# Kernel tuning notes

Measured on AMD Instinct MI355X. Metric: run time of the kernel, lower is better.

## Reference

```python
import jax, jax.numpy as jnp
import numpy as np

B, BARS, BEATS, FRAC = 64, 16, 4, 8
IN_F = 10 * 47 * 2  # 940
LIN_OUT = 100
BEAT_H = 16
BAR_H = 32


def _p(key, shape, scale=0.05):
    return jax.random.normal(key, shape, dtype=jnp.float32) * scale


def setup_inputs() -> dict:
    key = jax.random.key(0)
    ks = jax.random.split(key, 16)
    return {
        "channels": jax.random.normal(ks[0], (B, BARS, BEATS, FRAC, 10, 2, 47), dtype=jnp.float32),
        "lin_w": _p(ks[1], (LIN_OUT, IN_F)),
        "lin_b": _p(ks[2], (LIN_OUT,)),
        # beats LSTM (unidirectional), PyTorch gate order i,f,g,o
        "b_wih": _p(ks[3], (4 * BEAT_H, LIN_OUT)),
        "b_whh": _p(ks[4], (4 * BEAT_H, BEAT_H)),
        "b_bih": _p(ks[5], (4 * BEAT_H,)),
        "b_bhh": _p(ks[6], (4 * BEAT_H,)),
        # bars LSTM, bidirectional: forward (f_) and reverse (r_) directions
        "f_wih": _p(ks[7], (4 * BAR_H, BEAT_H)),
        "f_whh": _p(ks[8], (4 * BAR_H, BAR_H)),
        "f_bih": _p(ks[9], (4 * BAR_H,)),
        "f_bhh": _p(ks[10], (4 * BAR_H,)),
        "r_wih": _p(ks[11], (4 * BAR_H, BEAT_H)),
        "r_whh": _p(ks[12], (4 * BAR_H, BAR_H)),
        "r_bih": _p(ks[13], (4 * BAR_H,)),
        "r_bhh": _p(ks[14], (4 * BAR_H,)),
    }


def lstm(x, wih, whh, bih, bhh):
    """PyTorch-semantics LSTM, batch_first. x: [N, T, F] -> h_seq [N, T, H]."""
    N = x.shape[0]
    H = whh.shape[1]
    # precompute input contribution for all timesteps
    xg = jnp.einsum('ntf,gf->ntg', x, wih) + (bih + bhh)  # [N, T, 4H]

    def step(carry, xt):
        h, c = carry
        gates = xt + h @ whh.T  # [N, 4H]
        i, f, g, o = jnp.split(gates, 4, axis=-1)
        c = jax.nn.sigmoid(f) * c + jax.nn.sigmoid(i) * jnp.tanh(g)
        h = jax.nn.sigmoid(o) * jnp.tanh(c)
        return (h, c), h

    h0 = jnp.zeros((N, H), x.dtype)
    _, hs = jax.lax.scan(step, (h0, h0), jnp.swapaxes(xg, 0, 1))  # [T, N, H]
    return jnp.swapaxes(hs, 0, 1)


def bilstm(x, f_wih, f_whh, f_bih, f_bhh, r_wih, r_whh, r_bih, r_bhh):
    fwd = lstm(x, f_wih, f_whh, f_bih, f_bhh)
    bwd = jnp.flip(lstm(jnp.flip(x, axis=1), r_wih, r_whh, r_bih, r_bhh), axis=1)
    return jnp.concatenate([fwd, bwd], axis=-1)


def reference(channels, lin_w, lin_b,
              b_wih, b_whh, b_bih, b_bhh,
              f_wih, f_whh, f_bih, f_bhh,
              r_wih, r_whh, r_bih, r_bhh):
    # channels: [B, bars, beats, frac, 10, 2, 47]
    x = jnp.swapaxes(channels, -1, -2)  # [..., 10, 47, 2]
    x = x.reshape(*x.shape[:4], IN_F)   # squash dims 4..6 -> 940
    x = jax.nn.relu(x @ lin_w.T + lin_b)  # [B, bars, beats, frac, 100]

    # Distributed depth=2: fold (B, bars, beats) into batch, seq over frac
    xb = x.reshape(B * BARS * BEATS, FRAC, LIN_OUT)
    beats = lstm(xb, b_wih, b_whh, b_bih, b_bhh)
    beats = beats.reshape(B, BARS, BEATS, FRAC, BEAT_H)

    # last fraction hidden state, then Distributed depth=1 over beats axis
    xl = beats[:, :, :, -1].reshape(B * BARS, BEATS, BEAT_H)
    bars = bilstm(xl, f_wih, f_whh, f_bih, f_bhh, r_wih, r_whh, r_bih, r_bhh)
    bars = bars.reshape(B, BARS, BEATS, 2 * BAR_H)
    return beats, bars
```

## Files before the change

### kernel.cpp

```cpp
#include <hip/hip_runtime.h>
#include <hip/hip_bf16.h>

typedef float f32x4 __attribute__((ext_vector_type(4)));
typedef short bf16x8 __attribute__((ext_vector_type(8)));

#define MFMA16(a, b, c) __builtin_amdgcn_mfma_f32_16x16x32_bf16(a, b, c, 0, 0, 0)

constexpr int K1  = 940;
constexpr int KP2 = 1024;
constexpr int NP  = 112;
constexpr int OSL = 136;
constexpr int BSR = 136;
constexpr int BUFE = NP * BSR;

__device__ __forceinline__ float sigf(float x) { return 1.f / (1.f + __expf(-x)); }
__device__ __forceinline__ float tanhfast(float x) { return 2.f / (1.f + __expf(-2.f * x)) - 1.f; }

__device__ __forceinline__ short f2b(float x) {
  __hip_bfloat16 b = __float2bfloat16(x);
  return *reinterpret_cast<short*>(&b);
}

__global__ void prep_kernel(const float* __restrict__ lin_w,
                            const float* __restrict__ b_wih,
                            __hip_bfloat16* __restrict__ w2,
                            __hip_bfloat16* __restrict__ bw2) {
  int idx = blockIdx.x * 256 + threadIdx.x;
  if (idx < NP * KP2) {
    int n = idx >> 10, k = idx & 1023;
    float v = 0.f;
    if (n < 100 && k < K1) {
      int c10 = k / 94, rem = k - c10 * 94;
      int c2 = rem / 47, c47 = rem - c2 * 47;
      int f = c10 * 94 + c47 * 2 + c2;
      v = lin_w[n * K1 + f];
    }
    w2[idx] = __float2bfloat16(v);
  } else {
    int i2 = idx - NP * KP2;
    if (i2 < 64 * 128) {
      int g = i2 >> 7, k = i2 & 127;
      bw2[i2] = __float2bfloat16((k < 100) ? b_wih[g * 100 + k] : 0.f);
    }
  }
}

__global__ __launch_bounds__(256, 2)
void fused_encoder(const float* __restrict__ ch,
                   const __hip_bfloat16* __restrict__ w2,
                   const float* __restrict__ lin_b,
                   const __hip_bfloat16* __restrict__ bw2,
                   const float* __restrict__ bih,
                   const float* __restrict__ bhh,
                   const float* __restrict__ whh,
                   const float* __restrict__ fwih, const float* __restrict__ fwhh,
                   const float* __restrict__ fbih, const float* __restrict__ fbhh,
                   const float* __restrict__ rwih, const float* __restrict__ rwhh,
                   const float* __restrict__ rbih, const float* __restrict__ rbhh,
                   float* __restrict__ beats,
                   float* __restrict__ bars) {
  __shared__ __align__(16) char smem[2 * BUFE * 2];
  __hip_bfloat16* Bs    = reinterpret_cast<__hip_bfloat16*>(smem);
  __hip_bfloat16* out_s = reinterpret_cast<__hip_bfloat16*>(smem);
  float*          xg_s  = reinterpret_cast<float*>(smem + 17408);
  float (*hlast)[16]    = reinterpret_cast<float(*)[16]>(smem + 34048);
  float (*hb)[32]       = reinterpret_cast<float(*)[32]>(smem + 34560);
  float (*gact)[128]    = reinterpret_cast<float(*)[128]>(smem + 34816);

  const int tid = threadIdx.x;
  const int w = tid >> 6, lane = tid & 63;
  const int l16 = lane & 15, bq = lane >> 4;

  const int mbase = blockIdx.x * 64 + w * 16;
  const float* ar = ch + (long)(mbase + l16) * K1 + bq * 8;

  float lb[7];
#pragma unroll
  for (int nt = 0; nt < 7; ++nt) {
    int col = nt * 16 + l16;
    lb[nt] = (col < 100) ? lin_b[col] : 0.f;
  }

  auto mk = [&](float4 lo, float4 hi) -> bf16x8 {
    return bf16x8{f2b(lo.x), f2b(lo.y), f2b(lo.z), f2b(lo.w),
                  f2b(hi.x), f2b(hi.y), f2b(hi.z), f2b(hi.w)};
  };

  f32x4 acc[7] = {};
  float4 Ab[2][8];
  bf16x8 bst[8];

  const float4 f40{0.f, 0.f, 0.f, 0.f};
  auto ldA = [&](int c, float4* d) {
    const float* p = ar + c * 128;
    if (c < 7) {
#pragma unroll
      for (int ks = 0; ks < 4; ++ks) {
        d[2 * ks]     = *reinterpret_cast<const float4*>(p + ks * 32);
        d[2 * ks + 1] = *reinterpret_cast<const float4*>(p + ks * 32 + 4);
      }
    } else {
      d[0] = *reinterpret_cast<const float4*>(p);
      d[1] = *reinterpret_cast<const float4*>(p + 4);
      d[2] = (bq <= 1) ? *reinterpret_cast<const float4*>(p + 32) : f40;
      d[3] = (bq == 0) ? *reinterpret_cast<const float4*>(p + 36) : f40;
      d[4] = d[5] = d[6] = d[7] = f40;
    }
  };

  const int sn = tid >> 1, kh = (tid & 1) * 64;
  auto stageB_ld = [&](int c) {
    if (sn < NP) {
      const __hip_bfloat16* src = w2 + sn * KP2 + c * 128 + kh;
#pragma unroll
      for (int j = 0; j < 8; ++j)
        bst[j] = *reinterpret_cast<const bf16x8*>(src + j * 8);
    }
  };
  auto stageB_st = [&](int buf) {
    if (sn < NP) {
      __hip_bfloat16* dst = Bs + buf * BUFE + sn * BSR + kh;
#pragma unroll
      for (int j = 0; j < 8; ++j)
        *reinterpret_cast<bf16x8*>(dst + j * 8) = bst[j];
    }
  };

  stageB_ld(0);
  stageB_st(0);
  ldA(0, Ab[0]);
  __syncthreads();

  for (int c = 0; c < 8; ++c) {
    if (c < 7) {
      stageB_ld(c + 1);
      ldA(c + 1, Ab[(c + 1) & 1]);
    }
    const __hip_bfloat16* Bc = Bs + (c & 1) * BUFE;
    float4* A = Ab[c & 1];
#pragma unroll
    for (int ks = 0; ks < 4; ++ks) {
      bf16x8 bf[7];
#pragma unroll
      for (int nt = 0; nt < 7; ++nt)
        bf[nt] = *reinterpret_cast<const bf16x8*>(
            &Bc[(nt * 16 + l16) * BSR + ks * 32 + bq * 8]);
      bf16x8 a = mk(A[2 * ks], A[2 * ks + 1]);
#pragma unroll
      for (int nt = 0; nt < 7; ++nt) acc[nt] = MFMA16(a, bf[nt], acc[nt]);
    }
    if (c < 7) stageB_st((c + 1) & 1);
    __syncthreads();
  }

#pragma unroll
  for (int nt = 0; nt < 7; ++nt) {
    const int col = nt * 16 + l16;
#pragma unroll
    for (int r = 0; r < 4; ++r) {
      float v = fmaxf(acc[nt][r] + lb[nt], 0.f);
      out_s[(w * 16 + bq * 4 + r) * OSL + col] = __float2bfloat16((col < 100) ? v : 0.f);
    }
  }
#pragma unroll
  for (int r = 0; r < 4; ++r)
    out_s[(w * 16 + bq * 4 + r) * OSL + 112 + l16] = __float2bfloat16(0.f);

  {
    bf16x8 av[4];
#pragma unroll
    for (int s = 0; s < 4; ++s)
      av[s] = *reinterpret_cast<const bf16x8*>(&out_s[(w * 16 + l16) * OSL + s * 32 + bq * 8]);
    f32x4 xacc[4] = {};
#pragma unroll
    for (int gt = 0; gt < 4; ++gt) {
#pragma unroll
      for (int s = 0; s < 4; ++s) {
        bf16x8 b = *reinterpret_cast<const bf16x8*>(&bw2[(gt * 16 + l16) * 128 + s * 32 + bq * 8]);
        xacc[gt] = MFMA16(av[s], b, xacc[gt]);
      }
    }
#pragma unroll
    for (int gt = 0; gt < 4; ++gt) {
      const int gate = gt * 16 + l16;
      const float bias = bih[gate] + bhh[gate];
#pragma unroll
      for (int r = 0; r < 4; ++r)
        xg_s[(w * 16 + bq * 4 + r) * 65 + gate] = xacc[gt][r] + bias;
    }
  }

  {
    const int cell = lane & 15;
    float wr[16];
#pragma unroll
    for (int u = 0; u < 16; ++u) wr[u] = whh[lane * 16 + u];
    float xv0[8], xv1[8];
#pragma unroll
    for (int t = 0; t < 8; ++t) {
      xv0[t] = xg_s[(w * 16 + t) * 65 + lane];
      xv1[t] = xg_s[(w * 16 + 8 + t) * 65 + lane];
    }
    float h0[16], h1[16];
#pragma unroll
    for (int u = 0; u < 16; ++u) { h0[u] = 0.f; h1[u] = 0.f; }
    float c0 = 0.f, c1 = 0.f;
    const long sg0 = (long)blockIdx.x * 8 + 2 * w;
    const long sg1 = sg0 + 1;
#pragma unroll
    for (int t = 0; t < 8; ++t) {
      float p0 = xv0[t], p1 = xv1[t];
#pragma unroll
      for (int u = 0; u < 16; ++u) { p0 += wr[u] * h0[u]; p1 += wr[u] * h1[u]; }
      const bool istanh = (lane >= 32 && lane < 48);
      float a0 = istanh ? tanhfast(p0) : sigf(p0);
      float a1 = istanh ? tanhfast(p1) : sigf(p1);
      float gi0 = __shfl(a0, cell),      gi1 = __shfl(a1, cell);
      float gf0 = __shfl(a0, cell + 16), gf1 = __shfl(a1, cell + 16);
      float gg0 = __shfl(a0, cell + 32), gg1 = __shfl(a1, cell + 32);
      float go0 = __shfl(a0, cell + 48), go1 = __shfl(a1, cell + 48);
      c0 = gf0 * c0 + gi0 * gg0;
      c1 = gf1 * c1 + gi1 * gg1;
      float hn0 = go0 * tanhfast(c0);
      float hn1 = go1 * tanhfast(c1);
#pragma unroll
      for (int u = 0; u < 16; ++u) { h0[u] = __shfl(hn0, u); h1[u] = __shfl(hn1, u); }
      if (lane < 16) {
        beats[sg0 * 128 + t * 16 + lane] = hn0;
        beats[sg1 * 128 + t * 16 + lane] = hn1;
        if (t == 7) {
          hlast[2 * w][lane]     = hn0;
          hlast[2 * w + 1][lane] = hn1;
        }
      }
    }
  }
  __syncthreads();

  {
    const int dir = tid >> 7, g = tid & 127;
    const float* wihp = dir ? rwih : fwih;
    const float* whhp = dir ? rwhh : fwhh;
    const float bias = dir ? (rbih[g] + rbhh[g]) : (fbih[g] + fbhh[g]);
    float wi[16], wh[32];
#pragma unroll
    for (int u = 0; u < 16; ++u) wi[u] = wihp[g * 16 + u];
#pragma unroll
    for (int u = 0; u < 32; ++u) wh[u] = whhp[g * 32 + u];
    for (int b2 = 0; b2 < 2; ++b2) {
      const int n = blockIdx.x * 2 + b2;
      float c = 0.f;
      if (g < 32) hb[dir][g] = 0.f;
      __syncthreads();
      for (int t = 0; t < 4; ++t) {
        const int tt = dir ? (3 - t) : t;
        float pre = bias;
#pragma unroll
        for (int u = 0; u < 16; ++u) pre += wi[u] * hlast[b2 * 4 + tt][u];
#pragma unroll
        for (int u = 0; u < 32; ++u) pre += wh[u] * hb[dir][u];
        gact[dir][g] = (g >= 64 && g < 96) ? tanhfast(pre) : sigf(pre);
        __syncthreads();
        if (g < 32) {
          c = gact[dir][32 + g] * c + gact[dir][g] * gact[dir][64 + g];
          float hn = gact[dir][96 + g] * tanhfast(c);
          hb[dir][g] = hn;
          bars[(n * 4 + tt) * 64 + dir * 32 + g] = hn;
        }
        __syncthreads();
      }
    }
  }
}

extern "C" void kernel_launch(void* const* d_in, const int* in_sizes, int n_in,
                              void* d_out, int out_size, void* d_ws, size_t ws_size,
                              hipStream_t stream) {
  const float* ch    = (const float*)d_in[0];
  const float* lin_w = (const float*)d_in[1];
  const float* lin_b = (const float*)d_in[2];
  const float* b_wih = (const float*)d_in[3];
  const float* b_whh = (const float*)d_in[4];
  const float* b_bih = (const float*)d_in[5];
  const float* b_bhh = (const float*)d_in[6];
  const float* f_wih = (const float*)d_in[7];
  const float* f_whh = (const float*)d_in[8];
  const float* f_bih = (const float*)d_in[9];
  const float* f_bhh = (const float*)d_in[10];
  const float* r_wih = (const float*)d_in[11];
  const float* r_whh = (const float*)d_in[12];
  const float* r_bih = (const float*)d_in[13];
  const float* r_bhh = (const float*)d_in[14];

  char* ws = (char*)d_ws;
  __hip_bfloat16* w2  = (__hip_bfloat16*)ws;
  __hip_bfloat16* bw2 = (__hip_bfloat16*)(ws + 229376);
  float*          out = (float*)d_out;

  prep_kernel<<<480, 256, 0, stream>>>(lin_w, b_wih, w2, bw2);
  fused_encoder<<<512, 256, 0, stream>>>(ch, w2, lin_b, bw2, b_bih, b_bhh,
                                         b_whh,
                                         f_wih, f_whh, f_bih, f_bhh,
                                         r_wih, r_whh, r_bih, r_bhh,
                                         out, out + 524288);
}
```

Measured before the change: 227.9 us.

## Split fused encoder into split-K linear GEMM and separate LSTM kernel

Splits the fused kernel into two kernels. The first is a linear GEMM over 2048 blocks of 16 rows, where each of the four waves handles a quarter of K, loads B fragments straight from global memory with no LDS staging, and reduces the partial sums through shared memory. The second is a separate LSTM kernel that reads the bf16 linear activations from a workspace buffer. The goal is more parallelism and occupancy for the memory-bound GEMM, which reads about 123MB of input. The cost is an extra kernel launch and a global round-trip for the intermediate activations.

```diff
diff --git a/kernel.cpp b/kernel.cpp
--- a/kernel.cpp
+++ b/kernel.cpp
@@ -10,8 +10,6 @@
 constexpr int KP2 = 1024;
 constexpr int NP  = 112;
 constexpr int OSL = 136;
-constexpr int BSR = 136;
-constexpr int BUFE = NP * BSR;
 
 __device__ __forceinline__ float sigf(float x) { return 1.f / (1.f + __expf(-x)); }
 __device__ __forceinline__ float tanhfast(float x) { return 2.f / (1.f + __expf(-2.f * x)) - 1.f; }
@@ -19,6 +17,11 @@
 __device__ __forceinline__ short f2b(float x) {
   __hip_bfloat16 b = __float2bfloat16(x);
   return *reinterpret_cast<short*>(&b);
+}
+
+__device__ __forceinline__ bf16x8 mk8(float4 lo, float4 hi) {
+  return bf16x8{f2b(lo.x), f2b(lo.y), f2b(lo.z), f2b(lo.w),
+                f2b(hi.x), f2b(hi.y), f2b(hi.z), f2b(hi.w)};
 }
 
 __global__ void prep_kernel(const float* __restrict__ lin_w,
@@ -45,126 +48,110 @@
   }
 }
 
-__global__ __launch_bounds__(256, 2)
-void fused_encoder(const float* __restrict__ ch,
-                   const __hip_bfloat16* __restrict__ w2,
-                   const float* __restrict__ lin_b,
-                   const __hip_bfloat16* __restrict__ bw2,
-                   const float* __restrict__ bih,
-                   const float* __restrict__ bhh,
-                   const float* __restrict__ whh,
-                   const float* __restrict__ fwih, const float* __restrict__ fwhh,
-                   const float* __restrict__ fbih, const float* __restrict__ fbhh,
-                   const float* __restrict__ rwih, const float* __restrict__ rwhh,
-                   const float* __restrict__ rbih, const float* __restrict__ rbhh,
-                   float* __restrict__ beats,
-                   float* __restrict__ bars) {
-  __shared__ __align__(16) char smem[2 * BUFE * 2];
-  __hip_bfloat16* Bs    = reinterpret_cast<__hip_bfloat16*>(smem);
-  __hip_bfloat16* out_s = reinterpret_cast<__hip_bfloat16*>(smem);
-  float*          xg_s  = reinterpret_cast<float*>(smem + 17408);
-  float (*hlast)[16]    = reinterpret_cast<float(*)[16]>(smem + 34048);
-  float (*hb)[32]       = reinterpret_cast<float(*)[32]>(smem + 34560);
-  float (*gact)[128]    = reinterpret_cast<float(*)[128]>(smem + 34816);
-
+__global__ __launch_bounds__(256)
+void linear_gemm(const float* __restrict__ ch,
+                 const __hip_bfloat16* __restrict__ w2,
+                 const float* __restrict__ lin_b,
+                 __hip_bfloat16* __restrict__ out1) {
+  __shared__ float red[4][16][116];
   const int tid = threadIdx.x;
   const int w = tid >> 6, lane = tid & 63;
   const int l16 = lane & 15, bq = lane >> 4;
-
-  const int mbase = blockIdx.x * 64 + w * 16;
-  const float* ar = ch + (long)(mbase + l16) * K1 + bq * 8;
-
-  float lb[7];
-#pragma unroll
-  for (int nt = 0; nt < 7; ++nt) {
-    int col = nt * 16 + l16;
-    lb[nt] = (col < 100) ? lin_b[col] : 0.f;
-  }
-
-  auto mk = [&](float4 lo, float4 hi) -> bf16x8 {
-    return bf16x8{f2b(lo.x), f2b(lo.y), f2b(lo.z), f2b(lo.w),
-                  f2b(hi.x), f2b(hi.y), f2b(hi.z), f2b(hi.w)};
-  };
+  const int mbase = blockIdx.x * 16;
+  const int wkb = w * 256;
+  const float* ar = ch + (long)(mbase + l16) * K1 + wkb + bq * 8;
 
   f32x4 acc[7] = {};
-  float4 Ab[2][8];
-  bf16x8 bst[8];
-
-  const float4 f40{0.f, 0.f, 0.f, 0.f};
-  auto ldA = [&](int c, float4* d) {
-    const float* p = ar + c * 128;
-    if (c < 7) {
-#pragma unroll
-      for (int ks = 0; ks < 4; ++ks) {
-        d[2 * ks]     = *reinterpret_cast<const float4*>(p + ks * 32);
-        d[2 * ks + 1] = *reinterpret_cast<const float4*>(p + ks * 32 + 4);
-      }
-    } else {
+  float4 Aa[2][2];
+  bf16x8 Bb[2][7];
+
+  auto ldA = [&](int ks, float4* d) {
+    const float* p = ar + ks * 32;
+    const int k0 = wkb + ks * 32 + bq * 8;
+    if (k0 + 8 <= K1) {
       d[0] = *reinterpret_cast<const float4*>(p);
       d[1] = *reinterpret_cast<const float4*>(p + 4);
-      d[2] = (bq <= 1) ? *reinterpret_cast<const float4*>(p + 32) : f40;
-      d[3] = (bq == 0) ? *reinterpret_cast<const float4*>(p + 36) : f40;
-      d[4] = d[5] = d[6] = d[7] = f40;
+    } else {
+      float t[8];
+#pragma unroll
+      for (int j = 0; j < 8; ++j) t[j] = (k0 + j < K1) ? p[j] : 0.f;
+      d[0] = float4{t[0], t[1], t[2], t[3]};
+      d[1] = float4{t[4], t[5], t[6], t[7]};
     }
   };
-
-  const int sn = tid >> 1, kh = (tid & 1) * 64;
-  auto stageB_ld = [&](int c) {
-    if (sn < NP) {
-      const __hip_bfloat16* src = w2 + sn * KP2 + c * 128 + kh;
-#pragma unroll
-      for (int j = 0; j < 8; ++j)
-        bst[j] = *reinterpret_cast<const bf16x8*>(src + j * 8);
-    }
+  auto ldB = [&](int ks, bf16x8* d) {
+#pragma unroll
+    for (int nt = 0; nt < 7; ++nt)
+      d[nt] = *reinterpret_cast<const bf16x8*>(
+          &w2[(nt * 16 + l16) * KP2 + wkb + ks * 32 + bq * 8]);
   };
-  auto stageB_st = [&](int buf) {
-    if (sn < NP) {
-      __hip_bfloat16* dst = Bs + buf * BUFE + sn * BSR + kh;
-#pragma unroll
-      for (int j = 0; j < 8; ++j)
-        *reinterpret_cast<bf16x8*>(dst + j * 8) = bst[j];
-    }
-  };
-
-  stageB_ld(0);
-  stageB_st(0);
-  ldA(0, Ab[0]);
+
+  ldA(0, Aa[0]);
+  ldB(0, Bb[0]);
+#pragma unroll
+  for (int ks = 0; ks < 8; ++ks) {
+    if (ks < 7) { ldA(ks + 1, Aa[(ks + 1) & 1]); ldB(ks + 1, Bb[(ks + 1) & 1]); }
+    bf16x8 a = mk8(Aa[ks & 1][0], Aa[ks & 1][1]);
+#pragma unroll
+    for (int nt = 0; nt < 7; ++nt) acc[nt] = MFMA16(a, Bb[ks & 1][nt], acc[nt]);
+  }
+
+#pragma unroll
+  for (int nt = 0; nt < 7; ++nt)
+#pragma unroll
+    for (int r = 0; r < 4; ++r)
+      red[w][bq * 4 + r][nt * 16 + l16] = acc[nt][r];
   __syncthreads();
 
-  for (int c = 0; c < 8; ++c) {
-    if (c < 7) {
-      stageB_ld(c + 1);
-      ldA(c + 1, Ab[(c + 1) & 1]);
-    }
-    const __hip_bfloat16* Bc = Bs + (c & 1) * BUFE;
-    float4* A = Ab[c & 1];
-#pragma unroll
-    for (int ks = 0; ks < 4; ++ks) {
-      bf16x8 bf[7];
-#pragma unroll
-      for (int nt = 0; nt < 7; ++nt)
-        bf[nt] = *reinterpret_cast<const bf16x8*>(
-            &Bc[(nt * 16 + l16) * BSR + ks * 32 + bq * 8]);
-      bf16x8 a = mk(A[2 * ks], A[2 * ks + 1]);
-#pragma unroll
-      for (int nt = 0; nt < 7; ++nt) acc[nt] = MFMA16(a, bf[nt], acc[nt]);
-    }
-    if (c < 7) stageB_st((c + 1) & 1);
-    __syncthreads();
-  }
-
-#pragma unroll
-  for (int nt = 0; nt < 7; ++nt) {
-    const int col = nt * 16 + l16;
-#pragma unroll
-    for (int r = 0; r < 4; ++r) {
-      float v = fmaxf(acc[nt][r] + lb[nt], 0.f);
-      out_s[(w * 16 + bq * 4 + r) * OSL + col] = __float2bfloat16((col < 100) ? v : 0.f);
-    }
-  }
-#pragma unroll
-  for (int r = 0; r < 4; ++r)
-    out_s[(w * 16 + bq * 4 + r) * OSL + 112 + l16] = __float2bfloat16(0.f);
+#pragma unroll
+  for (int i = 0; i < 7; ++i) {
+    const int e = i * 256 + tid;
+    const int row = e / 112, col = e - row * 112;
+    float s = red[0][row][col] + red[1][row][col] +
+              red[2][row][col] + red[3][row][col];
+    float v = (col < 100) ? fmaxf(s + lin_b[col], 0.f) : 0.f;
+    out1[(long)(mbase + row) * 112 + col] = __float2bfloat16(v);
+  }
+}
+
+__global__ __launch_bounds__(256)
+void lstm_kernel(const __hip_bfloat16* __restrict__ out1,
+                 const __hip_bfloat16* __restrict__ bw2,
+                 const float* __restrict__ bih,
+                 const float* __restrict__ bhh,
+                 const float* __restrict__ whh,
+                 const float* __restrict__ fwih, const float* __restrict__ fwhh,
+                 const float* __restrict__ fbih, const float* __restrict__ fbhh,
+                 const float* __restrict__ rwih, const float* __restrict__ rwhh,
+                 const float* __restrict__ rbih, const float* __restrict__ rbhh,
+                 float* __restrict__ beats,
+                 float* __restrict__ bars) {
+  __shared__ __align__(16) __hip_bfloat16 out_s[64 * OSL];
+  __shared__ float xg_s[64 * 65];
+  __shared__ float hlast[8][16];
+  __shared__ float hb[2][32];
+  __shared__ float gact[2][128];
+
+  const int tid = threadIdx.x;
+  const int w = tid >> 6, lane = tid & 63;
+  const int l16 = lane & 15, bq = lane >> 4;
+  const long rbase = (long)blockIdx.x * 64;
+
+#pragma unroll
+  for (int it = 0; it < 4; ++it) {
+    const int e = it * 256 + tid;
+    if (e < 896) {
+      const int row = e / 14, g = e - row * 14;
+      *reinterpret_cast<bf16x8*>(&out_s[row * OSL + g * 8]) =
+          *reinterpret_cast<const bf16x8*>(&out1[(rbase + row) * 112 + g * 8]);
+    }
+  }
+  if (tid < 128) {
+    const int row = tid >> 1, c0 = 112 + (tid & 1) * 8;
+    bf16x8 z = {0, 0, 0, 0, 0, 0, 0, 0};
+    *reinterpret_cast<bf16x8*>(&out_s[row * OSL + c0]) = z;
+  }
+  __syncthreads();
 
   {
     bf16x8 av[4];
@@ -293,14 +280,15 @@
   const float* r_bhh = (const float*)d_in[14];
 
   char* ws = (char*)d_ws;
-  __hip_bfloat16* w2  = (__hip_bfloat16*)ws;
-  __hip_bfloat16* bw2 = (__hip_bfloat16*)(ws + 229376);
-  float*          out = (float*)d_out;
+  __hip_bfloat16* w2   = (__hip_bfloat16*)ws;
+  __hip_bfloat16* bw2  = (__hip_bfloat16*)(ws + 229376);
+  __hip_bfloat16* out1 = (__hip_bfloat16*)(ws + 245760);
+  float*          out  = (float*)d_out;
 
   prep_kernel<<<480, 256, 0, stream>>>(lin_w, b_wih, w2, bw2);
-  fused_encoder<<<512, 256, 0, stream>>>(ch, w2, lin_b, bw2, b_bih, b_bhh,
-                                         b_whh,
-                                         f_wih, f_whh, f_bih, f_bhh,
-                                         r_wih, r_whh, r_bih, r_bhh,
-                                         out, out + 524288);
-}
+  linear_gemm<<<2048, 256, 0, stream>>>(ch, w2, lin_b, out1);
+  lstm_kernel<<<512, 256, 0, stream>>>(out1, bw2, b_bih, b_bhh, b_whh,
+                                       f_wih, f_whh, f_bih, f_bhh,
+                                       r_wih, r_whh, r_bih, r_bhh,
+                                       out, out + 524288);
+}
```

Measured after the change: 275.6 us. +20.9%, slower.
